# Kernel optimization log

Hardware: AMD Instinct MI355X
Metric: run time of the kernel (lower is better)

Reference implementation:

```python
import jax, jax.numpy as jnp
import numpy as np

B, T, C = 2, 2048, 2048
H, KH, D = 16, 4, 128
EPS = 1e-6

def _rmsnorm(x, w, eps=EPS):
    # norm over last dim in fp32, matching torch RMSNorm
    xf = x.astype(jnp.float32)
    var = jnp.mean(xf * xf, axis=-1, keepdims=True)
    return w * (xf * jax.lax.rsqrt(var + eps)).astype(x.dtype)

def _rotate_half(x):
    x1, x2 = jnp.split(x, 2, axis=-1)
    return jnp.concatenate((-x2, x1), axis=-1)

def setup_inputs() -> dict:
    key = jax.random.key(0)
    ks = jax.random.split(key, 9)
    s = 0.02
    return {
        "x": jax.random.normal(ks[0], (B, T, C), jnp.float32),
        "cos": jax.random.uniform(ks[1], (B, T, D), jnp.float32),
        "sin": jax.random.uniform(ks[2], (B, T, D), jnp.float32),
        "Wq": jax.random.normal(ks[3], (H * D, C), jnp.float32) * s,
        "Wk": jax.random.normal(ks[4], (KH * D, C), jnp.float32) * s,
        "Wv": jax.random.normal(ks[5], (KH * D, C), jnp.float32) * s,
        "Wo": jax.random.normal(ks[6], (C, H * D), jnp.float32) * s,
        "q_norm_w": jnp.ones((D,), jnp.float32),
        "k_norm_w": jnp.ones((D,), jnp.float32),
    }

def reference(x, cos, sin, Wq, Wk, Wv, Wo, q_norm_w, k_norm_w):
    rep = H // KH
    # projections (torch Linear: y = x @ W.T)
    q = jnp.einsum('btc,oc->bto', x, Wq).reshape(B, T, H, D)
    k = jnp.einsum('btc,oc->bto', x, Wk).reshape(B, T, KH, D)
    v = jnp.einsum('btc,oc->bto', x, Wv).reshape(B, T, KH, D)
    # per-head RMSNorm on d_head
    q = _rmsnorm(q, q_norm_w)
    k = _rmsnorm(k, k_norm_w)
    # RoPE, cos/sin broadcast over heads
    c = cos[:, :, None, :]
    s = sin[:, :, None, :]
    q = q * c + _rotate_half(q) * s
    k = k * c + _rotate_half(k) * s
    # GQA attention without materializing repeated k/v
    qg = q.reshape(B, T, KH, rep, D)
    scale = 1.0 / jnp.sqrt(jnp.asarray(D, jnp.float32))
    scores = jnp.einsum('bqhrd,bkhd->bhrqk', qg, k) * scale  # (B,KH,rep,T,T)
    causal = jnp.tril(jnp.ones((T, T), bool))
    scores = jnp.where(causal, scores, jnp.finfo(scores.dtype).min)
    attn = jax.nn.softmax(scores, axis=-1)
    y = jnp.einsum('bhrqk,bkhd->bqhrd', attn, v)  # (B,T,KH,rep,D)
    y = y.reshape(B, T, H * D)
    return jnp.einsum('bto,co->btc', y, Wo)
```

## Files before the change

kernel.cpp:

```cpp
#include <hip/hip_runtime.h>


typedef __attribute__((ext_vector_type(8))) short bf16x8;
typedef __attribute__((ext_vector_type(4))) float f32x4;
typedef __attribute__((ext_vector_type(16))) float f32x16;

__device__ __forceinline__ unsigned short f2bf(float f) {
  union { float f; unsigned u; } v; v.f = f;
  unsigned u = v.u;
  u += 0x7fffu + ((u >> 16) & 1u);
  return (unsigned short)(u >> 16);
}
__device__ __forceinline__ float bf2f(unsigned short h) {
  union { unsigned u; float f; } v; v.u = ((unsigned)h) << 16;
  return v.f;
}
__device__ __forceinline__ unsigned cvtpk_bf16(float lo, float hi) {
  unsigned r;
  asm("v_cvt_pk_bf16_f32 %0, %1, %2" : "=v"(r) : "v"(lo), "v"(hi));
  return r;
}

__device__ __forceinline__ void gl_lds16(const void* g, void* l) {
  __builtin_amdgcn_global_load_lds(
      (const __attribute__((address_space(1))) unsigned int*)(unsigned long long)g,
      (__attribute__((address_space(3))) unsigned int*)(unsigned int)(unsigned long long)l,
      16, 0, 0);
}

__global__ void cvt_all(const float* __restrict__ x, const float* __restrict__ wq,
                        const float* __restrict__ wk, const float* __restrict__ wv,
                        const float* __restrict__ wo,
                        unsigned short* __restrict__ xb,
                        unsigned short* __restrict__ wcat,
                        unsigned short* __restrict__ wob) {
  const long nx = 2097152, nq = 1048576, nk = 262144;
  const long b1 = nx, b2 = nx + nq, b3 = b2 + nk, b4 = b3 + nk;
  const long tot = b4 + 1048576;
  long i = (long)blockIdx.x * blockDim.x + threadIdx.x;
  const long stride = (long)gridDim.x * blockDim.x;
  for (; i < tot; i += stride) {
    float4 vv; unsigned short* dst; long o;
    if (i < b1)      { vv = ((const float4*)x)[i];       dst = xb;   o = i; }
    else if (i < b2) { vv = ((const float4*)wq)[i - b1]; dst = wcat; o = i - b1; }
    else if (i < b3) { vv = ((const float4*)wk)[i - b2]; dst = wcat; o = (i - b2) + nq; }
    else if (i < b4) { vv = ((const float4*)wv)[i - b3]; dst = wcat; o = (i - b3) + nq + nk; }
    else             { vv = ((const float4*)wo)[i - b4]; dst = wob;  o = i - b4; }
    ushort4 u;
    u.x = f2bf(vv.x); u.y = f2bf(vv.y); u.z = f2bf(vv.z); u.w = f2bf(vv.w);
    ((ushort4*)dst)[o] = u;
  }
}

#define PH384(QM, QN, PF, GATE)                                               \
  {                                                                           \
    bf16x8 af[2][2], bg[3][2];                                                \
    _Pragma("unroll") for (int r = 0; r < 2; ++r) {                           \
      const char* pa = ldsc + curb + (((QM)*64 + (wm << 5) + r*16 + lr) << 7);\
      af[r][0] = *(const bf16x8*)(pa + csw0);                                 \
      af[r][1] = *(const bf16x8*)(pa + csw1);                                 \
    }                                                                         \
    _Pragma("unroll") for (int n = 0; n < 3; ++n) {                           \
      const char* pb = ldsc + curb + 16384 +                                  \
                       (((QN)*192 + wn*48 + n*16 + lr) << 7);                 \
      bg[n][0] = *(const bf16x8*)(pb + csw0);                                 \
      bg[n][1] = *(const bf16x8*)(pb + csw1);                                 \
    }                                                                         \
    PF                                                                        \
    __builtin_amdgcn_s_barrier();                                             \
    asm volatile("s_waitcnt lgkmcnt(0)" ::: "memory");                        \
    __builtin_amdgcn_sched_barrier(0);                                        \
    __builtin_amdgcn_s_setprio(1);                                            \
    _Pragma("unroll") for (int r = 0; r < 2; ++r)                             \
      _Pragma("unroll") for (int n = 0; n < 3; ++n) {                         \
        acc[(QM)*2+r][(QN)*3+n] = __builtin_amdgcn_mfma_f32_16x16x32_bf16(    \
            af[r][0], bg[n][0], acc[(QM)*2+r][(QN)*3+n], 0, 0, 0);            \
        acc[(QM)*2+r][(QN)*3+n] = __builtin_amdgcn_mfma_f32_16x16x32_bf16(    \
            af[r][1], bg[n][1], acc[(QM)*2+r][(QN)*3+n], 0, 0, 0);            \
      }                                                                       \
    __builtin_amdgcn_s_setprio(0);                                            \
    GATE                                                                      \
    __builtin_amdgcn_s_barrier();                                             \
  }

__global__ __launch_bounds__(512, 2)
void gemm384(const unsigned short* __restrict__ A,
             const unsigned short* __restrict__ Bm,
             unsigned short* __restrict__ Cp, int M, int N, int K) {
  __shared__ __align__(16) char ldsc[131072];
  const int nbn = N / 384;
  int wg = blockIdx.x;
  {
    const int cpx = (int)gridDim.x >> 3;
    wg = (wg & 7) * cpx + (wg >> 3);
  }
  const int m0 = (wg / nbn) << 7, n0 = (wg % nbn) * 384;
  const int tid = threadIdx.x;
  const int lane = tid & 63, wid = tid >> 6;
  const int lr = lane & 15, lg = lane >> 4;
  const int wm = wid >> 2, wn = wid & 3;
  const int csw0 = (lg << 4) ^ ((lr & 7) << 4);
  const int csw1 = (64 + (lg << 4)) ^ ((lr & 7) << 4);
  const int srowL = tid >> 3;
  const int scol = ((tid & 7) ^ (srowL & 7)) << 3;
  const unsigned short* Asrc = A + (size_t)(m0 + srowL) * K + scol;
  const unsigned short* Bsrc = Bm + (size_t)(n0 + srowL) * K + scol;
  const int sdst = wid << 10;
  const int NT = K >> 6;
  f32x4 acc[4][6] = {};
  gl_lds16(Asrc, ldsc + sdst);
  gl_lds16(Bsrc, ldsc + 16384 + sdst);
  gl_lds16(Bsrc + (size_t)64 * K, ldsc + 24576 + sdst);
  gl_lds16(Bsrc + (size_t)128 * K, ldsc + 32768 + sdst);
  gl_lds16(Asrc + (size_t)64 * K, ldsc + 8192 + sdst);
  gl_lds16(Bsrc + (size_t)192 * K, ldsc + 40960 + sdst);
  gl_lds16(Bsrc + (size_t)256 * K, ldsc + 49152 + sdst);
  gl_lds16(Bsrc + (size_t)320 * K, ldsc + 57344 + sdst);
  asm volatile("s_waitcnt vmcnt(4)" ::: "memory");
  __builtin_amdgcn_s_barrier();

  for (int t = 0; t < NT; ++t) {
    const int curb = (t & 1) << 16;
    const int nxtb = curb ^ 65536;
    const size_t kn = (size_t)(t + 1) << 6;
    const bool pf = (t + 1) < NT;
    PH384(0, 0,
      if (pf) { gl_lds16(Asrc + kn, ldsc + nxtb + sdst);
                gl_lds16(Bsrc + kn, ldsc + nxtb + 16384 + sdst); },
      if (pf) { asm volatile("s_waitcnt vmcnt(5)" ::: "memory"); }
      else    { asm volatile("s_waitcnt vmcnt(3)" ::: "memory"); } )
    PH384(1, 0,
      if (pf) { gl_lds16(Bsrc + (size_t)64 * K + kn, ldsc + nxtb + 24576 + sdst);
                gl_lds16(Bsrc + (size_t)128 * K + kn, ldsc + nxtb + 32768 + sdst); },
      if (pf) { asm volatile("s_waitcnt vmcnt(4)" ::: "memory"); }
      else    { asm volatile("s_waitcnt vmcnt(0)" ::: "memory"); } )
    PH384(0, 1,
      if (pf) { gl_lds16(Asrc + (size_t)64 * K + kn, ldsc + nxtb + 8192 + sdst);
                gl_lds16(Bsrc + (size_t)192 * K + kn, ldsc + nxtb + 40960 + sdst); }, )
    PH384(1, 1,
      if (pf) { gl_lds16(Bsrc + (size_t)256 * K + kn, ldsc + nxtb + 49152 + sdst);
                gl_lds16(Bsrc + (size_t)320 * K + kn, ldsc + nxtb + 57344 + sdst); },
      if (pf) { asm volatile("s_waitcnt vmcnt(4)" ::: "memory"); } )
  }
  #pragma unroll
  for (int mi = 0; mi < 4; ++mi) {
    const int mrow = m0 + ((mi >> 1) << 6) + (wm << 5) + ((mi & 1) << 4) + (lg << 2);
    #pragma unroll
    for (int ni = 0; ni < 6; ++ni) {
      const int ncol = n0 + (ni >= 3 ? 192 : 0) + wn * 48 + (ni % 3) * 16 + lr;
      #pragma unroll
      for (int i = 0; i < 4; ++i)
        Cp[(size_t)(mrow + i) * N + ncol] = f2bf(acc[mi][ni][i]);
    }
  }
}

__global__ __launch_bounds__(512, 2)
void gemm128n(const unsigned short* __restrict__ A,
              const unsigned short* __restrict__ Bm,
              float* __restrict__ Cp, int M, int N, int K) {
  __shared__ __align__(16) char ldsc[98304];
  const int nbn = N >> 8;
  int wg = blockIdx.x;
  { const int cpx = (int)gridDim.x >> 3;
    wg = (wg & 7) * cpx + (wg >> 3); }
  const int m0 = (wg / nbn) << 7, n0 = (wg % nbn) << 8;
  const int tid = threadIdx.x;
  const int lane = tid & 63, wid = tid >> 6;
  const int lr = lane & 15, lg = lane >> 4;
  const int wm = wid >> 1, wn = wid & 1;
  const int csw0 = (lg << 4) ^ ((lr & 7) << 4);
  const int csw1 = (64 + (lg << 4)) ^ ((lr & 7) << 4);
  const int srowL = tid >> 3;
  const int scol = ((tid & 7) ^ (srowL & 7)) << 3;
  const unsigned short* Asrc = A + (size_t)(m0 + srowL) * K + scol;
  const unsigned short* Bsrc = Bm + (size_t)(n0 + srowL) * K + scol;
  const int sdst = wid << 10;
  const int NT = K >> 6;
  f32x4 acc[2][8] = {};
  gl_lds16(Asrc, ldsc + sdst);
  gl_lds16(Asrc + (size_t)64 * K, ldsc + 8192 + sdst);
  gl_lds16(Bsrc, ldsc + 16384 + sdst);
  gl_lds16(Bsrc + (size_t)128 * K, ldsc + 24576 + sdst);
  gl_lds16(Bsrc + (size_t)64 * K, ldsc + 32768 + sdst);
  gl_lds16(Bsrc + (size_t)192 * K, ldsc + 40960 + sdst);
  asm volatile("s_waitcnt vmcnt(2)" ::: "memory");
  __builtin_amdgcn_s_barrier();

  for (int t = 0; t < NT; ++t) {
    const int curb = (t & 1) ? 49152 : 0;
    const int nxtb = 49152 - curb;
    const size_t kn = (size_t)(t + 1) << 6;
    const bool pf = (t + 1) < NT;
    #pragma unroll
    for (int ph = 0; ph < 2; ++ph) {
      bf16x8 af[2][2], bg[4][2];
      #pragma unroll
      for (int r = 0; r < 2; ++r) {
        const char* pa = ldsc + curb + (((wm << 5) + (r << 4) + lr) << 7);
        af[r][0] = *(const bf16x8*)(pa + csw0);
        af[r][1] = *(const bf16x8*)(pa + csw1);
      }
      #pragma unroll
      for (int n = 0; n < 4; ++n) {
        const char* pb = ldsc + curb + 16384 + ((ph << 1) + wn) * 8192 +
                         (((n << 4) + lr) << 7);
        bg[n][0] = *(const bf16x8*)(pb + csw0);
        bg[n][1] = *(const bf16x8*)(pb + csw1);
      }
      if (pf) {
        if (ph == 0) {
          gl_lds16(Asrc + kn, ldsc + nxtb + sdst);
          gl_lds16(Asrc + (size_t)64 * K + kn, ldsc + nxtb + 8192 + sdst);
          gl_lds16(Bsrc + kn, ldsc + nxtb + 16384 + sdst);
          gl_lds16(Bsrc + (size_t)128 * K + kn, ldsc + nxtb + 24576 + sdst);
        } else {
          gl_lds16(Bsrc + (size_t)64 * K + kn, ldsc + nxtb + 32768 + sdst);
          gl_lds16(Bsrc + (size_t)192 * K + kn, ldsc + nxtb + 40960 + sdst);
        }
      }
      __builtin_amdgcn_s_barrier();
      asm volatile("s_waitcnt lgkmcnt(0)" ::: "memory");
      __builtin_amdgcn_sched_barrier(0);
      __builtin_amdgcn_s_setprio(1);
      #pragma unroll
      for (int r = 0; r < 2; ++r)
        #pragma unroll
        for (int n = 0; n < 4; ++n) {
          acc[r][ph * 4 + n] = __builtin_amdgcn_mfma_f32_16x16x32_bf16(
              af[r][0], bg[n][0], acc[r][ph * 4 + n], 0, 0, 0);
          acc[r][ph * 4 + n] = __builtin_amdgcn_mfma_f32_16x16x32_bf16(
              af[r][1], bg[n][1], acc[r][ph * 4 + n], 0, 0, 0);
        }
      __builtin_amdgcn_s_setprio(0);
      if (ph == 0) {
        if (pf) { asm volatile("s_waitcnt vmcnt(4)" ::: "memory"); }
        else    { asm volatile("s_waitcnt vmcnt(0)" ::: "memory"); }
      } else {
        if (pf) { asm volatile("s_waitcnt vmcnt(2)" ::: "memory"); }
      }
      __builtin_amdgcn_s_barrier();
    }
  }
  #pragma unroll
  for (int r = 0; r < 2; ++r) {
    const int mrow = m0 + (wm << 5) + (r << 4) + (lg << 2);
    #pragma unroll
    for (int n = 0; n < 8; ++n) {
      const int ncol = n0 + (wn << 7) + (n << 4) + lr;
      #pragma unroll
      for (int i = 0; i < 4; ++i)
        Cp[(size_t)(mrow + i) * N + ncol] = acc[r][n][i];
    }
  }
}

__global__ __launch_bounds__(256)
void norm_rope(const unsigned short* __restrict__ qkv,
               const float* __restrict__ cosb, const float* __restrict__ sinb,
               const float* __restrict__ qw, const float* __restrict__ kw,
               unsigned short* __restrict__ Qb,
               unsigned short* __restrict__ Kb) {
  const int wv = threadIdx.x >> 6, l = threadIdx.x & 63;
  const int rr = blockIdx.x * 4 + wv;
  const int hh = rr % 20, bt = rr / 20;
  const bool isq = hh < 16;
  const ushort2 u = *(const ushort2*)(qkv + (size_t)bt * 3072 + (hh << 7) + 2 * l);
  const float v0 = bf2f(u.x), v1 = bf2f(u.y);
  float ss = v0 * v0 + v1 * v1;
  #pragma unroll
  for (int off = 1; off < 64; off <<= 1) ss += __shfl_xor(ss, off);
  const float rms = rsqrtf(ss * (1.0f / 128.0f) + 1e-6f);
  const float* w = isq ? qw : kw;
  const float2 w2 = *(const float2*)(w + 2 * l);
  const float n0 = v0 * rms * w2.x, n1 = v1 * rms * w2.y;
  const float sx0 = __shfl_xor(n0, 32), sx1 = __shfl_xor(n1, 32);
  const float p0 = (l < 32) ? -sx0 : sx0;
  const float p1 = (l < 32) ? -sx1 : sx1;
  const float2 c2 = *(const float2*)(cosb + (size_t)bt * 128 + 2 * l);
  const float2 s2 = *(const float2*)(sinb + (size_t)bt * 128 + 2 * l);
  const float qsc = isq ? 0.08838834764831845f : 1.0f;
  ushort2 o;
  o.x = f2bf((n0 * c2.x + p0 * s2.x) * qsc);
  o.y = f2bf((n1 * c2.y + p1 * s2.y) * qsc);
  const int b = bt >> 11, t = bt & 2047;
  if (isq)
    *(ushort2*)(Qb + (((size_t)(b * 16 + hh) * 2048 + t) << 7) + 2 * l) = o;
  else
    *(ushort2*)(Kb + (((size_t)(b * 4 + (hh - 16)) * 2048 + t) << 7) + 2 * l) = o;
}

__global__ __launch_bounds__(256)
void v_trans(const unsigned short* __restrict__ qkv, unsigned short* __restrict__ Vt) {
  __shared__ unsigned short tile[64][68];
  const int b = blockIdx.x >> 2, h = blockIdx.x & 3;
  const int t0 = blockIdx.y << 6, d0 = blockIdx.z << 6;
  const int tid = threadIdx.x;
  #pragma unroll
  for (int p = 0; p < 4; ++p) {
    const int idx = ((p << 8) + tid) << 2;
    const int r = idx >> 6, c = idx & 63;
    *(ushort4*)(&tile[r][c]) = *(const ushort4*)(
        qkv + (size_t)(b * 2048 + t0 + r) * 3072 + 2560 + (h << 7) + d0 + c);
  }
  __syncthreads();
  unsigned short* vbase = Vt + (size_t)((b * 4 + h) * 128 + d0) * 2048 + t0;
  #pragma unroll
  for (int p = 0; p < 4; ++p) {
    const int idx = ((p << 8) + tid) << 2;
    const int d = idx >> 6, tq = idx & 63;
    const int tin = (tq & 48) | ((tq & 8) >> 1) | ((tq & 4) << 1);
    ushort4 u;
    u.x = tile[tin + 0][d];
    u.y = tile[tin + 1][d];
    u.z = tile[tin + 2][d];
    u.w = tile[tin + 3][d];
    *(ushort4*)(vbase + ((size_t)d << 11) + tq) = u;
  }
}

__global__ __launch_bounds__(512)
void attn_fwd(const unsigned short* __restrict__ Qb,
              const unsigned short* __restrict__ Kb,
              const unsigned short* __restrict__ Vt,
              unsigned short* __restrict__ Y) {
  __shared__ __align__(16) char L[65536];
  const int bh = blockIdx.x;
  const int b = bh >> 4, h = bh & 15, hk = h >> 2;
  const int py = blockIdx.y;
  const int p = (py < 8) ? py : 23 - py;
  const int tid = threadIdx.x;
  const int lane = tid & 63, wid = tid >> 6;
  const int g = wid >> 2;
  const int wid2 = wid & 3;
  const int j = wid2 >> 1;
  const int qt = (p << 1) + j;
  const int sub = (wid2 & 1) << 5;
  const int l31 = lane & 31, hi = lane >> 5;
  const int swb = (lane & 7) << 4;
  char* KsC = L + g * 32768;
  char* VsC = KsC + 16384;
  const unsigned short* Kp = Kb + (size_t)(b * 4 + hk) * 2048 * 128;
  const unsigned short* Vp = Vt + (size_t)(b * 4 + hk) * 128 * 2048;
  const int qg = qt * 64 + sub + l31;
  const unsigned short* Qp = Qb + (size_t)((b * 16 + h) * 2048 + qg) * 128;
  bf16x8 aq[8];
  #pragma unroll
  for (int ks = 0; ks < 8; ++ks)
    aq[ks] = *(const bf16x8*)(Qp + (ks << 4) + (hi << 3));
  float m_i = -1e30f, l_i = 0.f;
  f32x16 acc[4] = {};
  const int kr_in = (lane >> 4), kcb = (lane & 15) << 4;
  const int vr_in = (lane >> 3), vcb = (lane & 7) << 4;
  const int nkb = (p << 1) + 2;
  const int nit = (nkb + 1) >> 1;

  for (int it = 0; it < nit; ++it) {
    const int kb = 2 * it + g;
    const bool act = kb < nkb;
    if (act) {
      const int k0 = kb << 6;
      #pragma unroll
      for (int i = 0; i < 4; ++i) {
        const int c = (wid2 << 2) + i;
        { const int r = (c << 2) + kr_in;
          const int sw = kcb ^ ((r & 7) << 4);
          gl_lds16(Kp + (size_t)(k0 + r) * 128 + (sw >> 1), KsC + (c << 10)); }
        { const int r = (c << 3) + vr_in;
          const int sw = vcb ^ ((r & 7) << 4);
          gl_lds16(Vp + (size_t)r * 2048 + k0 + (sw >> 1), VsC + (c << 10)); }
      }
    }
    __syncthreads();
    if (act && kb <= qt) {
      const int k0 = kb << 6;
      f32x16 s[2] = {};
      __builtin_amdgcn_s_setprio(1);
      #pragma unroll
      for (int sblk = 0; sblk < 2; ++sblk) {
        const int row = (sblk << 5) + l31;
        #pragma unroll
        for (int ks = 0; ks < 8; ++ks) {
          const bf16x8 bk = *(const bf16x8*)(
              KsC + (row << 8) + (((ks << 5) + (hi << 4)) ^ swb));
          s[sblk] = __builtin_amdgcn_mfma_f32_32x32x16_bf16(bk, aq[ks], s[sblk], 0, 0, 0);
        }
      }
      __builtin_amdgcn_s_setprio(0);
      if (kb == qt) {
        #pragma unroll
        for (int sblk = 0; sblk < 2; ++sblk)
          #pragma unroll
          for (int r = 0; r < 16; ++r) {
            const int kv = k0 + (sblk << 5) + (r & 3) + ((r >> 2) << 3) + (hi << 2);
            if (kv > qg) s[sblk][r] = -1e30f;
          }
      }
      float mx = s[0][0];
      #pragma unroll
      for (int sblk = 0; sblk < 2; ++sblk)
        #pragma unroll
        for (int r = 0; r < 16; ++r) mx = fmaxf(mx, s[sblk][r]);
      mx = fmaxf(mx, __shfl_xor(mx, 32));
      if (!__all(mx <= m_i + 8.0f)) {
        const float mn = fmaxf(m_i, mx);
        const float r = __expf(m_i - mn);
        m_i = mn;
        l_i *= r;
        #pragma unroll
        for (int d = 0; d < 4; ++d)
          #pragma unroll
          for (int i = 0; i < 16; ++i) acc[d][i] *= r;
      }
      float se = 0.f;
      unsigned pk[16];
      #pragma unroll
      for (int t2 = 0; t2 < 16; ++t2) {
        const int f0 = 2 * t2, f1 = 2 * t2 + 1;
        const float e0 = __expf(s[f0 >> 4][f0 & 15] - m_i);
        const float e1 = __expf(s[f1 >> 4][f1 & 15] - m_i);
        se += e0 + e1;
        pk[t2] = cvtpk_bf16(e0, e1);
      }
      se += __shfl_xor(se, 32);
      l_i += se;
      __builtin_amdgcn_s_setprio(1);
      #pragma unroll
      for (int dblk = 0; dblk < 4; ++dblk) {
        const int row = (dblk << 5) + l31;
        #pragma unroll
        for (int cp = 0; cp < 4; ++cp) {
          const bf16x8 va = *(const bf16x8*)(
              VsC + (row << 7) + (((cp << 5) + (hi << 4)) ^ swb));
          union { unsigned u[4]; bf16x8 v; } pb;
          pb.u[0] = pk[cp * 4 + 0]; pb.u[1] = pk[cp * 4 + 1];
          pb.u[2] = pk[cp * 4 + 2]; pb.u[3] = pk[cp * 4 + 3];
          acc[dblk] = __builtin_amdgcn_mfma_f32_32x32x16_bf16(va, pb.v, acc[dblk], 0, 0, 0);
        }
      }
      __builtin_amdgcn_s_setprio(0);
    }
    __syncthreads();
  }

  float* cb = (float*)L;
  #pragma unroll
  for (int jj = 0; jj < 2; ++jj) {
    const int base = (((wid2 & 1) << 6) + lane) * 66;
    if (g == 1 && j == jj) {
      #pragma unroll
      for (int d = 0; d < 4; ++d)
        #pragma unroll
        for (int i = 0; i < 16; ++i) cb[base + d * 16 + i] = acc[d][i];
      cb[base + 64] = m_i;
      cb[base + 65] = l_i;
    }
    __syncthreads();
    if (g == 0 && j == jj) {
      const float m1 = cb[base + 64], l1v = cb[base + 65];
      const float m = fmaxf(m_i, m1);
      const float e0 = __expf(m_i - m), e1 = __expf(m1 - m);
      const float inv = 1.0f / (l_i * e0 + l1v * e1);
      unsigned short* Yp = Y + (((size_t)b * 2048 + qg) * 16 + h) * 128;
      #pragma unroll
      for (int dblk = 0; dblk < 4; ++dblk) {
        #pragma unroll
        for (int qd = 0; qd < 4; ++qd) {
          ushort4 o;
          o.x = f2bf((acc[dblk][qd * 4 + 0] * e0 + cb[base + dblk * 16 + qd * 4 + 0] * e1) * inv);
          o.y = f2bf((acc[dblk][qd * 4 + 1] * e0 + cb[base + dblk * 16 + qd * 4 + 1] * e1) * inv);
          o.z = f2bf((acc[dblk][qd * 4 + 2] * e0 + cb[base + dblk * 16 + qd * 4 + 2] * e1) * inv);
          o.w = f2bf((acc[dblk][qd * 4 + 3] * e0 + cb[base + dblk * 16 + qd * 4 + 3] * e1) * inv);
          *(ushort4*)(Yp + (dblk << 5) + (qd << 3) + (hi << 2)) = o;
        }
      }
    }
    __syncthreads();
  }
}

extern "C" void kernel_launch(void* const* d_in, const int* in_sizes, int n_in,
                              void* d_out, int out_size, void* d_ws, size_t ws_size,
                              hipStream_t stream) {
  const float* x    = (const float*)d_in[0];
  const float* cosb = (const float*)d_in[1];
  const float* sinb = (const float*)d_in[2];
  const float* Wq   = (const float*)d_in[3];
  const float* Wk   = (const float*)d_in[4];
  const float* Wv   = (const float*)d_in[5];
  const float* Wo   = (const float*)d_in[6];
  const float* qw   = (const float*)d_in[7];
  const float* kw   = (const float*)d_in[8];
  char* ws = (char*)d_ws;
  unsigned short* xb   = (unsigned short*)(ws);
  unsigned short* Wcat = (unsigned short*)(ws + (16ull << 20));
  unsigned short* Wob  = (unsigned short*)(ws + (28ull << 20));
  unsigned short* qkv  = (unsigned short*)(ws + (36ull << 20));
  unsigned short* Qb   = (unsigned short*)(ws + (60ull << 20));
  unsigned short* Kb   = (unsigned short*)(ws + (76ull << 20));
  unsigned short* Vt   = (unsigned short*)(ws + (80ull << 20));

  cvt_all<<<2048, 256, 0, stream>>>(x, Wq, Wk, Wv, Wo, xb, Wcat, Wob);

  gemm384<<<256, 512, 0, stream>>>(xb, Wcat, qkv, 4096, 3072, 2048);
  norm_rope<<<2 * 2048 * 20 / 4, 256, 0, stream>>>(qkv, cosb, sinb, qw, kw, Qb, Kb);
  v_trans<<<dim3(8, 32, 2), 256, 0, stream>>>(qkv, Vt);
  attn_fwd<<<dim3(32, 16), 512, 0, stream>>>(Qb, Kb, Vt, xb);
  gemm128n<<<256, 512, 0, stream>>>(xb, Wob, (float*)d_out, 4096, 2048, 2048);
}
```

Before: 199.2 us.

## Switch projection GEMMs to 32x32x16 MFMA with single-barrier K-step pipeline

```diff
diff --git a/kernel.cpp b/kernel.cpp
--- a/kernel.cpp
+++ b/kernel.cpp
@@ -52,37 +52,6 @@
   }
 }
 
-#define PH384(QM, QN, PF, GATE)                                               \
-  {                                                                           \
-    bf16x8 af[2][2], bg[3][2];                                                \
-    _Pragma("unroll") for (int r = 0; r < 2; ++r) {                           \
-      const char* pa = ldsc + curb + (((QM)*64 + (wm << 5) + r*16 + lr) << 7);\
-      af[r][0] = *(const bf16x8*)(pa + csw0);                                 \
-      af[r][1] = *(const bf16x8*)(pa + csw1);                                 \
-    }                                                                         \
-    _Pragma("unroll") for (int n = 0; n < 3; ++n) {                           \
-      const char* pb = ldsc + curb + 16384 +                                  \
-                       (((QN)*192 + wn*48 + n*16 + lr) << 7);                 \
-      bg[n][0] = *(const bf16x8*)(pb + csw0);                                 \
-      bg[n][1] = *(const bf16x8*)(pb + csw1);                                 \
-    }                                                                         \
-    PF                                                                        \
-    __builtin_amdgcn_s_barrier();                                             \
-    asm volatile("s_waitcnt lgkmcnt(0)" ::: "memory");                        \
-    __builtin_amdgcn_sched_barrier(0);                                        \
-    __builtin_amdgcn_s_setprio(1);                                            \
-    _Pragma("unroll") for (int r = 0; r < 2; ++r)                             \
-      _Pragma("unroll") for (int n = 0; n < 3; ++n) {                         \
-        acc[(QM)*2+r][(QN)*3+n] = __builtin_amdgcn_mfma_f32_16x16x32_bf16(    \
-            af[r][0], bg[n][0], acc[(QM)*2+r][(QN)*3+n], 0, 0, 0);            \
-        acc[(QM)*2+r][(QN)*3+n] = __builtin_amdgcn_mfma_f32_16x16x32_bf16(    \
-            af[r][1], bg[n][1], acc[(QM)*2+r][(QN)*3+n], 0, 0, 0);            \
-      }                                                                       \
-    __builtin_amdgcn_s_setprio(0);                                            \
-    GATE                                                                      \
-    __builtin_amdgcn_s_barrier();                                             \
-  }
-
 __global__ __launch_bounds__(512, 2)
 void gemm384(const unsigned short* __restrict__ A,
              const unsigned short* __restrict__ Bm,
@@ -90,33 +59,38 @@
   __shared__ __align__(16) char ldsc[131072];
   const int nbn = N / 384;
   int wg = blockIdx.x;
-  {
-    const int cpx = (int)gridDim.x >> 3;
-    wg = (wg & 7) * cpx + (wg >> 3);
-  }
+  { const int cpx = (int)gridDim.x >> 3;
+    wg = (wg & 7) * cpx + (wg >> 3); }
   const int m0 = (wg / nbn) << 7, n0 = (wg % nbn) * 384;
   const int tid = threadIdx.x;
   const int lane = tid & 63, wid = tid >> 6;
-  const int lr = lane & 15, lg = lane >> 4;
+  const int l31 = lane & 31, hi = lane >> 5;
   const int wm = wid >> 2, wn = wid & 3;
-  const int csw0 = (lg << 4) ^ ((lr & 7) << 4);
-  const int csw1 = (64 + (lg << 4)) ^ ((lr & 7) << 4);
+  const int swb = (lane & 7) << 4;
+  int aoff[2], boff[3];
+  #pragma unroll
+  for (int am = 0; am < 2; ++am) {
+    const int r = wm * 64 + am * 32 + l31;
+    aoff[am] = ((r >> 6) << 13) + ((r & 63) << 7);
+  }
+  #pragma unroll
+  for (int bn = 0; bn < 3; ++bn) {
+    const int r = wn * 96 + bn * 32 + l31;
+    boff[bn] = 16384 + ((r >> 6) << 13) + ((r & 63) << 7);
+  }
   const int srowL = tid >> 3;
   const int scol = ((tid & 7) ^ (srowL & 7)) << 3;
   const unsigned short* Asrc = A + (size_t)(m0 + srowL) * K + scol;
   const unsigned short* Bsrc = Bm + (size_t)(n0 + srowL) * K + scol;
   const int sdst = wid << 10;
   const int NT = K >> 6;
-  f32x4 acc[4][6] = {};
+  f32x16 acc[2][3] = {};
   gl_lds16(Asrc, ldsc + sdst);
-  gl_lds16(Bsrc, ldsc + 16384 + sdst);
-  gl_lds16(Bsrc + (size_t)64 * K, ldsc + 24576 + sdst);
-  gl_lds16(Bsrc + (size_t)128 * K, ldsc + 32768 + sdst);
   gl_lds16(Asrc + (size_t)64 * K, ldsc + 8192 + sdst);
-  gl_lds16(Bsrc + (size_t)192 * K, ldsc + 40960 + sdst);
-  gl_lds16(Bsrc + (size_t)256 * K, ldsc + 49152 + sdst);
-  gl_lds16(Bsrc + (size_t)320 * K, ldsc + 57344 + sdst);
-  asm volatile("s_waitcnt vmcnt(4)" ::: "memory");
+  #pragma unroll
+  for (int c = 0; c < 6; ++c)
+    gl_lds16(Bsrc + (size_t)(64 * c) * K, ldsc + 16384 + c * 8192 + sdst);
+  asm volatile("s_waitcnt vmcnt(0)" ::: "memory");
   __builtin_amdgcn_s_barrier();
 
   for (int t = 0; t < NT; ++t) {
@@ -124,33 +98,56 @@
     const int nxtb = curb ^ 65536;
     const size_t kn = (size_t)(t + 1) << 6;
     const bool pf = (t + 1) < NT;
-    PH384(0, 0,
-      if (pf) { gl_lds16(Asrc + kn, ldsc + nxtb + sdst);
-                gl_lds16(Bsrc + kn, ldsc + nxtb + 16384 + sdst); },
-      if (pf) { asm volatile("s_waitcnt vmcnt(5)" ::: "memory"); }
-      else    { asm volatile("s_waitcnt vmcnt(3)" ::: "memory"); } )
-    PH384(1, 0,
-      if (pf) { gl_lds16(Bsrc + (size_t)64 * K + kn, ldsc + nxtb + 24576 + sdst);
-                gl_lds16(Bsrc + (size_t)128 * K + kn, ldsc + nxtb + 32768 + sdst); },
-      if (pf) { asm volatile("s_waitcnt vmcnt(4)" ::: "memory"); }
-      else    { asm volatile("s_waitcnt vmcnt(0)" ::: "memory"); } )
-    PH384(0, 1,
-      if (pf) { gl_lds16(Asrc + (size_t)64 * K + kn, ldsc + nxtb + 8192 + sdst);
-                gl_lds16(Bsrc + (size_t)192 * K + kn, ldsc + nxtb + 40960 + sdst); }, )
-    PH384(1, 1,
-      if (pf) { gl_lds16(Bsrc + (size_t)256 * K + kn, ldsc + nxtb + 49152 + sdst);
-                gl_lds16(Bsrc + (size_t)320 * K + kn, ldsc + nxtb + 57344 + sdst); },
-      if (pf) { asm volatile("s_waitcnt vmcnt(4)" ::: "memory"); } )
-  }
-  #pragma unroll
-  for (int mi = 0; mi < 4; ++mi) {
-    const int mrow = m0 + ((mi >> 1) << 6) + (wm << 5) + ((mi & 1) << 4) + (lg << 2);
     #pragma unroll
-    for (int ni = 0; ni < 6; ++ni) {
-      const int ncol = n0 + (ni >= 3 ? 192 : 0) + wn * 48 + (ni % 3) * 16 + lr;
-      #pragma unroll
-      for (int i = 0; i < 4; ++i)
-        Cp[(size_t)(mrow + i) * N + ncol] = f2bf(acc[mi][ni][i]);
+    for (int half = 0; half < 2; ++half) {
+      bf16x8 af[2][2], bg[3][2];
+      #pragma unroll
+      for (int am = 0; am < 2; ++am)
+        #pragma unroll
+        for (int tt = 0; tt < 2; ++tt)
+          af[am][tt] = *(const bf16x8*)(ldsc + curb + aoff[am] +
+              ((((half * 2 + tt) << 5) + (hi << 4)) ^ swb));
+      #pragma unroll
+      for (int bn = 0; bn < 3; ++bn)
+        #pragma unroll
+        for (int tt = 0; tt < 2; ++tt)
+          bg[bn][tt] = *(const bf16x8*)(ldsc + curb + boff[bn] +
+              ((((half * 2 + tt) << 5) + (hi << 4)) ^ swb));
+      if (half == 0 && pf) {
+        gl_lds16(Asrc + kn, ldsc + nxtb + sdst);
+        gl_lds16(Asrc + (size_t)64 * K + kn, ldsc + nxtb + 8192 + sdst);
+        #pragma unroll
+        for (int c = 0; c < 6; ++c)
+          gl_lds16(Bsrc + (size_t)(64 * c) * K + kn,
+                   ldsc + nxtb + 16384 + c * 8192 + sdst);
+      }
+      asm volatile("s_waitcnt lgkmcnt(0)" ::: "memory");
+      __builtin_amdgcn_sched_barrier(0);
+      __builtin_amdgcn_s_setprio(1);
+      #pragma unroll
+      for (int am = 0; am < 2; ++am)
+        #pragma unroll
+        for (int bn = 0; bn < 3; ++bn)
+          #pragma unroll
+          for (int tt = 0; tt < 2; ++tt)
+            acc[am][bn] = __builtin_amdgcn_mfma_f32_32x32x16_bf16(
+                af[am][tt], bg[bn][tt], acc[am][bn], 0, 0, 0);
+      __builtin_amdgcn_s_setprio(0);
+    }
+    asm volatile("s_waitcnt vmcnt(0)" ::: "memory");
+    __builtin_amdgcn_s_barrier();
+  }
+  #pragma unroll
+  for (int am = 0; am < 2; ++am) {
+    const int mrowb = m0 + wm * 64 + am * 32 + (hi << 2);
+    #pragma unroll
+    for (int bn = 0; bn < 3; ++bn) {
+      const int ncol = n0 + wn * 96 + bn * 32 + l31;
+      #pragma unroll
+      for (int qd = 0; qd < 4; ++qd)
+        #pragma unroll
+        for (int i = 0; i < 4; ++i)
+          Cp[(size_t)(mrowb + 8 * qd + i) * N + ncol] = f2bf(acc[am][bn][qd * 4 + i]);
     }
   }
 }
@@ -167,24 +164,33 @@
   const int m0 = (wg / nbn) << 7, n0 = (wg % nbn) << 8;
   const int tid = threadIdx.x;
   const int lane = tid & 63, wid = tid >> 6;
-  const int lr = lane & 15, lg = lane >> 4;
-  const int wm = wid >> 1, wn = wid & 1;
-  const int csw0 = (lg << 4) ^ ((lr & 7) << 4);
-  const int csw1 = (64 + (lg << 4)) ^ ((lr & 7) << 4);
+  const int l31 = lane & 31, hi = lane >> 5;
+  const int wm = wid >> 2, wn = wid & 3;
+  const int swb = (lane & 7) << 4;
+  int aoff[2], boff[2];
+  #pragma unroll
+  for (int am = 0; am < 2; ++am) {
+    const int r = wm * 64 + am * 32 + l31;
+    aoff[am] = ((r >> 6) << 13) + ((r & 63) << 7);
+  }
+  #pragma unroll
+  for (int bn = 0; bn < 2; ++bn) {
+    const int r = wn * 64 + bn * 32 + l31;
+    boff[bn] = 16384 + ((r >> 6) << 13) + ((r & 63) << 7);
+  }
   const int srowL = tid >> 3;
   const int scol = ((tid & 7) ^ (srowL & 7)) << 3;
   const unsigned short* Asrc = A + (size_t)(m0 + srowL) * K + scol;
   const unsigned short* Bsrc = Bm + (size_t)(n0 + srowL) * K + scol;
   const int sdst = wid << 10;
   const int NT = K >> 6;
-  f32x4 acc[2][8] = {};
+  f32x16 acc[2][2] = {};
   gl_lds16(Asrc, ldsc + sdst);
   gl_lds16(Asrc + (size_t)64 * K, ldsc + 8192 + sdst);
-  gl_lds16(Bsrc, ldsc + 16384 + sdst);
-  gl_lds16(Bsrc + (size_t)128 * K, ldsc + 24576 + sdst);
-  gl_lds16(Bsrc + (size_t)64 * K, ldsc + 32768 + sdst);
-  gl_lds16(Bsrc + (size_t)192 * K, ldsc + 40960 + sdst);
-  asm volatile("s_waitcnt vmcnt(2)" ::: "memory");
+  #pragma unroll
+  for (int c = 0; c < 4; ++c)
+    gl_lds16(Bsrc + (size_t)(64 * c) * K, ldsc + 16384 + c * 8192 + sdst);
+  asm volatile("s_waitcnt vmcnt(0)" ::: "memory");
   __builtin_amdgcn_s_barrier();
 
   for (int t = 0; t < NT; ++t) {
@@ -193,64 +199,55 @@
     const size_t kn = (size_t)(t + 1) << 6;
     const bool pf = (t + 1) < NT;
     #pragma unroll
-    for (int ph = 0; ph < 2; ++ph) {
-      bf16x8 af[2][2], bg[4][2];
-      #pragma unroll
-      for (int r = 0; r < 2; ++r) {
-        const char* pa = ldsc + curb + (((wm << 5) + (r << 4) + lr) << 7);
-        af[r][0] = *(const bf16x8*)(pa + csw0);
-        af[r][1] = *(const bf16x8*)(pa + csw1);
-      }
-      #pragma unroll
-      for (int n = 0; n < 4; ++n) {
-        const char* pb = ldsc + curb + 16384 + ((ph << 1) + wn) * 8192 +
-                         (((n << 4) + lr) << 7);
-        bg[n][0] = *(const bf16x8*)(pb + csw0);
-        bg[n][1] = *(const bf16x8*)(pb + csw1);
-      }
-      if (pf) {
-        if (ph == 0) {
-          gl_lds16(Asrc + kn, ldsc + nxtb + sdst);
-          gl_lds16(Asrc + (size_t)64 * K + kn, ldsc + nxtb + 8192 + sdst);
-          gl_lds16(Bsrc + kn, ldsc + nxtb + 16384 + sdst);
-          gl_lds16(Bsrc + (size_t)128 * K + kn, ldsc + nxtb + 24576 + sdst);
-        } else {
-          gl_lds16(Bsrc + (size_t)64 * K + kn, ldsc + nxtb + 32768 + sdst);
-          gl_lds16(Bsrc + (size_t)192 * K + kn, ldsc + nxtb + 40960 + sdst);
-        }
-      }
-      __builtin_amdgcn_s_barrier();
+    for (int half = 0; half < 2; ++half) {
+      bf16x8 af[2][2], bg[2][2];
+      #pragma unroll
+      for (int am = 0; am < 2; ++am)
+        #pragma unroll
+        for (int tt = 0; tt < 2; ++tt)
+          af[am][tt] = *(const bf16x8*)(ldsc + curb + aoff[am] +
+              ((((half * 2 + tt) << 5) + (hi << 4)) ^ swb));
+      #pragma unroll
+      for (int bn = 0; bn < 2; ++bn)
+        #pragma unroll
+        for (int tt = 0; tt < 2; ++tt)
+          bg[bn][tt] = *(const bf16x8*)(ldsc + curb + boff[bn] +
+              ((((half * 2 + tt) << 5) + (hi << 4)) ^ swb));
+      if (half == 0 && pf) {
+        gl_lds16(Asrc + kn, ldsc + nxtb + sdst);
+        gl_lds16(Asrc + (size_t)64 * K + kn, ldsc + nxtb + 8192 + sdst);
+        #pragma unroll
+        for (int c = 0; c < 4; ++c)
+          gl_lds16(Bsrc + (size_t)(64 * c) * K + kn,
+                   ldsc + nxtb + 16384 + c * 8192 + sdst);
+      }
       asm volatile("s_waitcnt lgkmcnt(0)" ::: "memory");
       __builtin_amdgcn_sched_barrier(0);
       __builtin_amdgcn_s_setprio(1);
       #pragma unroll
-      for (int r = 0; r < 2; ++r)
-        #pragma unroll
-        for (int n = 0; n < 4; ++n) {
-          acc[r][ph * 4 + n] = __builtin_amdgcn_mfma_f32_16x16x32_bf16(
-              af[r][0], bg[n][0], acc[r][ph * 4 + n], 0, 0, 0);
-          acc[r][ph * 4 + n] = __builtin_amdgcn_mfma_f32_16x16x32_bf16(
-              af[r][1], bg[n][1], acc[r][ph * 4 + n], 0, 0, 0);
-        }
+      for (int am = 0; am < 2; ++am)
+        #pragma unroll
+        for (int bn = 0; bn < 2; ++bn)
+          #pragma unroll
+          for (int tt = 0; tt < 2; ++tt)
+            acc[am][bn] = __builtin_amdgcn_mfma_f32_32x32x16_bf16(
+                af[am][tt], bg[bn][tt], acc[am][bn], 0, 0, 0);
       __builtin_amdgcn_s_setprio(0);
-      if (ph == 0) {
-        if (pf) { asm volatile("s_waitcnt vmcnt(4)" ::: "memory"); }
-        else    { asm volatile("s_waitcnt vmcnt(0)" ::: "memory"); }
-      } else {
-        if (pf) { asm volatile("s_waitcnt vmcnt(2)" ::: "memory"); }
-      }
-      __builtin_amdgcn_s_barrier();
-    }
-  }
-  #pragma unroll
-  for (int r = 0; r < 2; ++r) {
-    const int mrow = m0 + (wm << 5) + (r << 4) + (lg << 2);
+    }
+    asm volatile("s_waitcnt vmcnt(0)" ::: "memory");
+    __builtin_amdgcn_s_barrier();
+  }
+  #pragma unroll
+  for (int am = 0; am < 2; ++am) {
+    const int mrowb = m0 + wm * 64 + am * 32 + (hi << 2);
     #pragma unroll
-    for (int n = 0; n < 8; ++n) {
-      const int ncol = n0 + (wn << 7) + (n << 4) + lr;
-      #pragma unroll
-      for (int i = 0; i < 4; ++i)
-        Cp[(size_t)(mrow + i) * N + ncol] = acc[r][n][i];
+    for (int bn = 0; bn < 2; ++bn) {
+      const int ncol = n0 + wn * 64 + bn * 32 + l31;
+      #pragma unroll
+      for (int qd = 0; qd < 4; ++qd)
+        #pragma unroll
+        for (int i = 0; i < 4; ++i)
+          Cp[(size_t)(mrowb + 8 * qd + i) * N + ncol] = acc[am][bn][qd * 4 + i];
     }
   }
 }
```

Result: faster. 194.5 us (-2.3%).
